# Kernel tuning notes

Hardware: AMD Instinct MI355X
Metric: run time of the kernel (lower is better)

Reference implementation:

```python
import jax, jax.numpy as jnp
import numpy as np

D_MODEL = 1024
NUM_HEADS_Q = 16
NUM_HEADS_KV = 1
D_HEAD = D_MODEL // NUM_HEADS_Q  # 64
KV_DIM = D_HEAD * NUM_HEADS_KV   # 64


def setup_inputs() -> dict:
    key = jax.random.key(0)
    ks = jax.random.split(key, 9)
    b, n = 4, 2048
    s_in = 1.0 / np.sqrt(D_MODEL)
    s_o = 1.0 / np.sqrt(D_MODEL)
    return {
        "x": jax.random.normal(ks[0], (b, n, D_MODEL), jnp.float32),
        # weights stored as [in, out] (= torch Linear weight transposed)
        "W_q": jax.random.uniform(ks[1], (D_MODEL, D_MODEL), jnp.float32, -s_in, s_in),
        "b_q": jax.random.uniform(ks[2], (D_MODEL,), jnp.float32, -s_in, s_in),
        "W_k": jax.random.uniform(ks[3], (D_MODEL, KV_DIM), jnp.float32, -s_in, s_in),
        "b_k": jax.random.uniform(ks[4], (KV_DIM,), jnp.float32, -s_in, s_in),
        "W_v": jax.random.uniform(ks[5], (D_MODEL, KV_DIM), jnp.float32, -s_in, s_in),
        "b_v": jax.random.uniform(ks[6], (KV_DIM,), jnp.float32, -s_in, s_in),
        "W_o": jax.random.uniform(ks[7], (D_MODEL, D_MODEL), jnp.float32, -s_o, s_o),
        "b_o": jax.random.uniform(ks[8], (D_MODEL,), jnp.float32, -s_o, s_o),
    }


def reference(x, W_q, b_q, W_k, b_k, W_v, b_v, W_o, b_o):
    b, n, d_model = x.shape
    # projections
    q = (x @ W_q + b_q).reshape(b, n, NUM_HEADS_Q, D_HEAD).transpose(0, 2, 1, 3)  # [b,hq,n,dh]
    k = (x @ W_k + b_k).reshape(b, n, NUM_HEADS_KV, D_HEAD).transpose(0, 2, 1, 3)  # [b,hkv,n,dh]
    v = (x @ W_v + b_v).reshape(b, n, NUM_HEADS_KV, D_HEAD).transpose(0, 2, 1, 3)
    # MQA: single KV head broadcast over query heads via einsum broadcasting
    scale = 1.0 / np.sqrt(D_HEAD).astype(np.float32)
    # scores [b,hq,n,n]; k/v have hkv=1, broadcast over hq
    scores = jnp.einsum("bhqd,bknd->bhqn", q, k)[..., 0, :, :][:, :, None] if False else None
    # cleaner: squeeze kv head (num_heads_kv == 1)
    k1 = k[:, 0]  # [b,n,dh]
    v1 = v[:, 0]  # [b,n,dh]
    scores = jnp.einsum("bhqd,bkd->bhqk", q, k1) * scale  # [b,hq,n,n]
    attn = jax.nn.softmax(scores, axis=-1)
    out = jnp.einsum("bhqk,bkd->bhqd", attn, v1)  # [b,hq,n,dh]
    out = out.transpose(0, 2, 1, 3).reshape(b, n, d_model)
    return out @ W_o + b_o
```

## Files before the change

### kernel.cpp

```cpp
#include <hip/hip_runtime.h>

using bf16x8 = __attribute__((ext_vector_type(8))) short;
using f32x4  = __attribute__((ext_vector_type(4))) float;
using f32x16 = __attribute__((ext_vector_type(16))) float;
using u32x2  = __attribute__((ext_vector_type(2))) unsigned int;
using u32x4  = __attribute__((ext_vector_type(4))) unsigned int;

__device__ __forceinline__ unsigned short f2bf(float f) {
  unsigned int u = __float_as_uint(f);
  u = u + 0x7fffu + ((u >> 16) & 1u);
  return (unsigned short)(u >> 16);
}

#if __has_builtin(__builtin_amdgcn_exp2f)
#define EXP2(x) __builtin_amdgcn_exp2f(x)
#else
#define EXP2(x) __expf((x) * 0.69314718056f)
#endif

__device__ __forceinline__ unsigned int cvt_pk_bf16(float lo, float hi) {
  unsigned int r;
  asm("v_cvt_pk_bf16_f32 %0, %1, %2" : "=v"(r) : "v"(lo), "v"(hi));
  return r;
}

#define GLL16(SRC, DST) __builtin_amdgcn_global_load_lds( \
    (const __attribute__((address_space(1))) unsigned int*)(SRC), \
    (__attribute__((address_space(3))) unsigned int*)(DST), 16, 0, 0)

__global__ void cvt_x_kernel(const float* __restrict__ x, unsigned short* __restrict__ xb, int n4) {
  int i = blockIdx.x * blockDim.x + threadIdx.x;
  if (i >= n4) return;
  const float4 v = reinterpret_cast<const float4*>(x)[i];
  ushort2 o0 = { f2bf(v.x), f2bf(v.y) };
  ushort2 o1 = { f2bf(v.z), f2bf(v.w) };
  reinterpret_cast<ushort2*>(xb)[2 * i]     = o0;
  reinterpret_cast<ushort2*>(xb)[2 * i + 1] = o1;
}

__global__ __launch_bounds__(256) void cvt_wt_kernel(
    const float* __restrict__ W, unsigned short* __restrict__ Wt, int N, int K) {
  __shared__ float tile[32][33];
  const int n0 = blockIdx.x * 32, k0 = blockIdx.y * 32;
  const int tx = threadIdx.x & 31, ty = threadIdx.x >> 5;
  #pragma unroll
  for (int i = 0; i < 32; i += 8)
    tile[ty + i][tx] = W[(size_t)(k0 + ty + i) * N + n0 + tx];
  __syncthreads();
  #pragma unroll
  for (int i = 0; i < 32; i += 8)
    Wt[(size_t)(n0 + ty + i) * K + k0 + tx] = f2bf(tile[tx][ty + i]);
}

template<int MODE>
__global__ __launch_bounds__(256) void gemm_kernel(
    const unsigned short* __restrict__ A, const unsigned short* __restrict__ Bt,
    const float* __restrict__ bias0, const float* __restrict__ bias1,
    const float* __restrict__ bias2,
    void* __restrict__ out0, void* __restrict__ out1, void* __restrict__ out2,
    int K, int N) {
  __shared__ __align__(16) unsigned short alds[2][128 * 32];
  __shared__ __align__(16) unsigned short blds[2][128 * 32];

  const int t    = threadIdx.x;
  const int lane = t & 63;
  const int wid  = t >> 6;
  const int lr = lane & 15, lg = lane >> 4;
  const int row0 = blockIdx.x * 128;
  const int col0 = blockIdx.y * 128;

  const size_t ldb = (size_t)K * 2;
  const char* Ag = (const char*)A  + (size_t)(row0 + (t >> 2)) * ldb + ((t & 3) << 4);
  const char* Bg = (const char*)Bt + (size_t)(col0 + (t >> 2)) * ldb + ((t & 3) << 4);
  char* adst = (char*)alds[0] + wid * 1024;
  char* bdst = (char*)blds[0] + wid * 1024;

  auto stage = [&](int buf, int k0) {
    const size_t kb = (size_t)k0 * 2;
    #pragma unroll
    for (int c = 0; c < 2; ++c) {
      GLL16(Ag + (size_t)c * 64 * ldb + kb, adst + buf * 8192 + c * 4096);
      GLL16(Bg + (size_t)c * 64 * ldb + kb, bdst + buf * 8192 + c * 4096);
    }
  };

  f32x4 acc[4][4];
  #pragma unroll
  for (int i = 0; i < 4; ++i)
    #pragma unroll
    for (int j = 0; j < 4; ++j)
      #pragma unroll
      for (int r = 0; r < 4; ++r) acc[i][j][r] = 0.f;

  stage(0, 0);
  __syncthreads();

  for (int step = 0; step < 32; ++step) {
    const int cur = step & 1;
    if (step < 31) stage(cur ^ 1, (step + 1) * 32);

    const char* ab = (const char*)alds[cur] + (wid >> 1) * 4096;
    const char* bb = (const char*)blds[cur] + (wid & 1) * 4096;
    bf16x8 am[4], bn[4];
    #pragma unroll
    for (int i = 0; i < 4; ++i)
      am[i] = *reinterpret_cast<const bf16x8*>(ab + (i * 16 + lr) * 64 + lg * 16);
    #pragma unroll
    for (int j = 0; j < 4; ++j)
      bn[j] = *reinterpret_cast<const bf16x8*>(bb + (j * 16 + lr) * 64 + lg * 16);
    #pragma unroll
    for (int i = 0; i < 4; ++i)
      #pragma unroll
      for (int j = 0; j < 4; ++j)
        acc[i][j] = __builtin_amdgcn_mfma_f32_16x16x32_bf16(am[i], bn[j], acc[i][j], 0, 0, 0);

    __syncthreads();
  }

  const int wrow0 = row0 + (wid >> 1) * 64;
  const int wcol0 = col0 + (wid & 1) * 64;
  #pragma unroll
  for (int i = 0; i < 4; ++i) {
    #pragma unroll
    for (int j = 0; j < 4; ++j) {
      const int col = wcol0 + j * 16 + lr;
      float bias;
      if constexpr (MODE == 0)
        bias = (col < 1024) ? bias0[col] : ((col < 1088) ? bias1[col - 1024] : bias2[col - 1088]);
      else
        bias = bias0[col];
      #pragma unroll
      for (int r = 0; r < 4; ++r) {
        const int row = wrow0 + i * 16 + lg * 4 + r;
        float v = acc[i][j][r] + bias;
        if constexpr (MODE == 0) {
          const int b = row >> 11, n = row & 2047;
          if (col < 1024) {
            v *= 0.180336880111f;
            const int h = col >> 6, d = col & 63;
            ((unsigned short*)out0)[(((b * 16 + h) * 2048) + n) * 64 + d] = f2bf(v);
          } else if (col < 1088) {
            ((unsigned short*)out1)[row * 64 + (col - 1024)] = f2bf(v);
          } else {
            const int np = (n & ~15) | (n & 3) | ((n & 4) << 1) | ((n & 8) >> 1);
            ((unsigned short*)out2)[(b * 64 + (col - 1088)) * 2048 + np] = f2bf(v);
          }
        } else {
          ((float*)out0)[(size_t)row * N + col] = v;
        }
      }
    }
  }
}

__global__ __launch_bounds__(512, 4) void attn_kernel(
    const unsigned short* __restrict__ Q,
    const unsigned short* __restrict__ Kb,
    const unsigned short* __restrict__ Vt,
    unsigned short* __restrict__ Ao) {
  __shared__ __align__(16) unsigned short klds[2][128 * 64];
  __shared__ __align__(16) unsigned short vlds[2][64 * 128];

  const int lane = threadIdx.x & 63;
  const int wid  = threadIdx.x >> 6;
  const int la = lane & 31, hi = lane >> 5;
  const int swz = (la & 7) << 4;
  const int bh = blockIdx.y, b = bh >> 4, h = bh & 15;
  const int q0 = blockIdx.x * 256 + wid * 32;

  const unsigned short* Qb = Q + (size_t)bh * 2048 * 64;
  const char* Kbase = (const char*)(Kb + (size_t)b * 2048 * 64);
  const char* Vbase = (const char*)(Vt + (size_t)b * 64 * 2048);

  const int srowK  = lane >> 3;
  const int schnkK = (lane & 7) ^ srowK;
  const int koff0 = (wid * 16 + 0 + srowK) * 128 + schnkK * 16;
  const int koff1 = (wid * 16 + 8 + srowK) * 128 + schnkK * 16;
  const int srowV = lane >> 4;
  const int voff0 = (wid * 8 + 0 + srowV) * 4096 + ((lane & 15) ^ ((0 + srowV) & 7)) * 16;
  const int voff1 = (wid * 8 + 4 + srowV) * 4096 + ((lane & 15) ^ ((4 + srowV) & 7)) * 16;
  char* kB = (char*)klds[0] + wid * 2048;
  char* vB = (char*)vlds[0] + wid * 2048;

  auto stage = [&](int buf, int p) {
    const size_t kgb = (size_t)p * 16384;
    const size_t vgb = (size_t)p * 256;
    GLL16(Kbase + kgb + koff0, kB + buf * 16384);
    GLL16(Kbase + kgb + koff1, kB + buf * 16384 + 1024);
    GLL16(Vbase + vgb + voff0, vB + buf * 16384);
    GLL16(Vbase + vgb + voff1, vB + buf * 16384 + 1024);
  };

  bf16x8 qa[4];
  #pragma unroll
  for (int kc = 0; kc < 4; ++kc)
    qa[kc] = *reinterpret_cast<const bf16x8*>(&Qb[(q0 + la) * 64 + kc * 16 + hi * 8]);

  float lsum = 0.f;
  f32x16 o[2];
  #pragma unroll
  for (int dt = 0; dt < 2; ++dt)
    #pragma unroll
    for (int r = 0; r < 16; ++r) o[dt][r] = 0.f;

  stage(0, 0);
  __syncthreads();

  for (int p = 0; p < 16; ++p) {
    const int cur = p & 1;
    if (p < 15) stage(cur ^ 1, p + 1);

    const char* kb8 = (const char*)klds[cur];
    const char* vb8 = (const char*)vlds[cur];

    #pragma unroll
    for (int ct = 0; ct < 4; ++ct) {
      f32x16 s;
      #pragma unroll
      for (int r = 0; r < 16; ++r) s[r] = 0.f;
      #pragma unroll
      for (int kc = 0; kc < 4; ++kc) {
        const bf16x8 kf = *reinterpret_cast<const bf16x8*>(
            kb8 + ((ct * 32 + la) << 7) + ((((kc << 1) + hi) << 4) ^ swz));
        s = __builtin_amdgcn_mfma_f32_32x32x16_bf16(kf, qa[kc], s, 0, 0, 0);
      }

      unsigned int W[4][2];
      float ps = 0.f;
      #pragma unroll
      for (int r2 = 0; r2 < 4; ++r2) {
        const float p0 = EXP2(s[r2 * 4 + 0]);
        const float p1 = EXP2(s[r2 * 4 + 1]);
        const float p2 = EXP2(s[r2 * 4 + 2]);
        const float p3 = EXP2(s[r2 * 4 + 3]);
        ps += (p0 + p1) + (p2 + p3);
        W[r2][0] = cvt_pk_bf16(p0, p1);
        W[r2][1] = cvt_pk_bf16(p2, p3);
      }
      lsum += ps;

      #pragma unroll
      for (int ks = 0; ks < 2; ++ks) {
        u32x4 pwv;
        pwv[0] = W[2 * ks][0];
        pwv[1] = W[2 * ks][1];
        pwv[2] = W[2 * ks + 1][0];
        pwv[3] = W[2 * ks + 1][1];
        const bf16x8 pb = __builtin_bit_cast(bf16x8, pwv);
        #pragma unroll
        for (int dt = 0; dt < 2; ++dt) {
          const bf16x8 vf = *reinterpret_cast<const bf16x8*>(
              vb8 + ((dt * 32 + la) << 8) + (((((ct * 2 + ks) << 1) + hi) << 4) ^ swz));
          o[dt] = __builtin_amdgcn_mfma_f32_32x32x16_bf16(vf, pb, o[dt], 0, 0, 0);
        }
      }
    }

    __syncthreads();
  }

  lsum += __shfl_xor(lsum, 32);
  const float inv = 1.f / lsum;
  const size_t rowoff = (size_t)(b * 2048 + q0 + la) * 1024 + h * 64 + hi * 4;
  #pragma unroll
  for (int dt = 0; dt < 2; ++dt) {
    #pragma unroll
    for (int r2 = 0; r2 < 4; ++r2) {
      u32x2 w;
      w[0] = cvt_pk_bf16(o[dt][r2 * 4 + 0] * inv, o[dt][r2 * 4 + 1] * inv);
      w[1] = cvt_pk_bf16(o[dt][r2 * 4 + 2] * inv, o[dt][r2 * 4 + 3] * inv);
      *(u32x2*)(Ao + rowoff + dt * 32 + r2 * 8) = w;
    }
  }
}

extern "C" void kernel_launch(void* const* d_in, const int* in_sizes, int n_in,
                              void* d_out, int out_size, void* d_ws, size_t ws_size,
                              hipStream_t stream) {
  const float* x  = (const float*)d_in[0];
  const float* Wq = (const float*)d_in[1];
  const float* bq = (const float*)d_in[2];
  const float* Wk = (const float*)d_in[3];
  const float* bk = (const float*)d_in[4];
  const float* Wv = (const float*)d_in[5];
  const float* bv = (const float*)d_in[6];
  const float* Wo = (const float*)d_in[7];
  const float* bo = (const float*)d_in[8];
  float* out = (float*)d_out;

  char* ws = (char*)d_ws;
  size_t off = 0;
  auto alloc = [&](size_t bytes) -> void* {
    void* p = ws + off;
    off += (bytes + 255) & ~(size_t)255;
    return p;
  };
  unsigned short* xb    = (unsigned short*)alloc((size_t)8192 * 1024 * 2);
  unsigned short* wqkvt = (unsigned short*)alloc((size_t)1152 * 1024 * 2);
  unsigned short* wot   = (unsigned short*)alloc((size_t)1024 * 1024 * 2);
  unsigned short* qb    = (unsigned short*)alloc((size_t)8192 * 1024 * 2);
  unsigned short* kb    = (unsigned short*)alloc((size_t)8192 * 64 * 2);
  unsigned short* vt    = (unsigned short*)alloc((size_t)4 * 64 * 2048 * 2);
  unsigned short* ao    = (unsigned short*)alloc((size_t)8192 * 1024 * 2);

  cvt_x_kernel<<<8192, 256, 0, stream>>>(x, xb, 8192 * 1024 / 4);
  cvt_wt_kernel<<<dim3(32, 32), 256, 0, stream>>>(Wq, wqkvt, 1024, 1024);
  cvt_wt_kernel<<<dim3(2, 32), 256, 0, stream>>>(Wk, wqkvt + (size_t)1024 * 1024, 64, 1024);
  cvt_wt_kernel<<<dim3(2, 32), 256, 0, stream>>>(Wv, wqkvt + (size_t)1088 * 1024, 64, 1024);
  cvt_wt_kernel<<<dim3(32, 32), 256, 0, stream>>>(Wo, wot, 1024, 1024);

  gemm_kernel<0><<<dim3(64, 9), 256, 0, stream>>>(xb, wqkvt, bq, bk, bv, qb, kb, vt, 1024, 1152);
  attn_kernel<<<dim3(8, 64), 512, 0, stream>>>(qb, kb, vt, ao);
  gemm_kernel<2><<<dim3(64, 8), 256, 0, stream>>>(ao, wot, bo, nullptr, nullptr, out, nullptr, nullptr, 1024, 1024);
}
```

Measured before the change: 161.5 us.

## Fuse conversion kernels, software-pipeline QK and PV with priorities, relax attention occupancy

The five fp32-to-bf16 conversion launches are merged into one kernel that dispatches on block index, removing launch overhead. Inside attention, the QK^T MFMA for the next column tile is issued before the exp/PV of the previous one, with s_setprio raised around MFMA bursts so matrix work overlaps the exp work of other waves. The launch-bounds minimum blocks is lowered from 4 to 2, letting the compiler use more registers for the extra live score tile, at the cost of possibly lower occupancy.

```diff
diff --git a/kernel.cpp b/kernel.cpp
--- a/kernel.cpp
+++ b/kernel.cpp
@@ -28,20 +28,29 @@
     (const __attribute__((address_space(1))) unsigned int*)(SRC), \
     (__attribute__((address_space(3))) unsigned int*)(DST), 16, 0, 0)
 
-__global__ void cvt_x_kernel(const float* __restrict__ x, unsigned short* __restrict__ xb, int n4) {
-  int i = blockIdx.x * blockDim.x + threadIdx.x;
-  if (i >= n4) return;
-  const float4 v = reinterpret_cast<const float4*>(x)[i];
-  ushort2 o0 = { f2bf(v.x), f2bf(v.y) };
-  ushort2 o1 = { f2bf(v.z), f2bf(v.w) };
-  reinterpret_cast<ushort2*>(xb)[2 * i]     = o0;
-  reinterpret_cast<ushort2*>(xb)[2 * i + 1] = o1;
-}
-
-__global__ __launch_bounds__(256) void cvt_wt_kernel(
-    const float* __restrict__ W, unsigned short* __restrict__ Wt, int N, int K) {
+__global__ __launch_bounds__(256) void cvt_all_kernel(
+    const float* __restrict__ x, unsigned short* __restrict__ xb,
+    const float* __restrict__ Wq, const float* __restrict__ Wk,
+    const float* __restrict__ Wv, const float* __restrict__ Wo,
+    unsigned short* __restrict__ wqkvt, unsigned short* __restrict__ wot) {
   __shared__ float tile[32][33];
-  const int n0 = blockIdx.x * 32, k0 = blockIdx.y * 32;
+  const int bx = blockIdx.x;
+  if (bx < 8192) {
+    const int i = bx * 256 + threadIdx.x;
+    const float4 v = reinterpret_cast<const float4*>(x)[i];
+    ushort2 o0 = { f2bf(v.x), f2bf(v.y) };
+    ushort2 o1 = { f2bf(v.z), f2bf(v.w) };
+    reinterpret_cast<ushort2*>(xb)[2 * i]     = o0;
+    reinterpret_cast<ushort2*>(xb)[2 * i + 1] = o1;
+    return;
+  }
+  const float* W; unsigned short* Wt; int N, bi;
+  if (bx < 9216)      { W = Wq; Wt = wqkvt;                        N = 1024; bi = bx - 8192; }
+  else if (bx < 9280) { W = Wk; Wt = wqkvt + (size_t)1024 * 1024;  N = 64;   bi = bx - 9216; }
+  else if (bx < 9344) { W = Wv; Wt = wqkvt + (size_t)1088 * 1024;  N = 64;   bi = bx - 9280; }
+  else                { W = Wo; Wt = wot;                          N = 1024; bi = bx - 9344; }
+  const int nb = N >> 5;
+  const int n0 = (bi % nb) * 32, k0 = (bi / nb) * 32;
   const int tx = threadIdx.x & 31, ty = threadIdx.x >> 5;
   #pragma unroll
   for (int i = 0; i < 32; i += 8)
@@ -49,7 +58,7 @@
   __syncthreads();
   #pragma unroll
   for (int i = 0; i < 32; i += 8)
-    Wt[(size_t)(n0 + ty + i) * K + k0 + tx] = f2bf(tile[tx][ty + i]);
+    Wt[(size_t)(n0 + ty + i) * 1024 + k0 + tx] = f2bf(tile[tx][ty + i]);
 }
 
 template<int MODE>
@@ -153,7 +162,7 @@
   }
 }
 
-__global__ __launch_bounds__(512, 4) void attn_kernel(
+__global__ __launch_bounds__(512, 2) void attn_kernel(
     const unsigned short* __restrict__ Q,
     const unsigned short* __restrict__ Kb,
     const unsigned short* __restrict__ Vt,
@@ -213,18 +222,22 @@
     const char* kb8 = (const char*)klds[cur];
     const char* vb8 = (const char*)vlds[cur];
 
-    #pragma unroll
-    for (int ct = 0; ct < 4; ++ct) {
+    auto QKc = [&](int ct) -> f32x16 {
       f32x16 s;
       #pragma unroll
       for (int r = 0; r < 16; ++r) s[r] = 0.f;
+      __builtin_amdgcn_s_setprio(1);
       #pragma unroll
       for (int kc = 0; kc < 4; ++kc) {
         const bf16x8 kf = *reinterpret_cast<const bf16x8*>(
             kb8 + ((ct * 32 + la) << 7) + ((((kc << 1) + hi) << 4) ^ swz));
         s = __builtin_amdgcn_mfma_f32_32x32x16_bf16(kf, qa[kc], s, 0, 0, 0);
       }
-
+      __builtin_amdgcn_s_setprio(0);
+      return s;
+    };
+
+    auto ExpPV = [&](int ct, const f32x16& s) {
       unsigned int W[4][2];
       float ps = 0.f;
       #pragma unroll
@@ -238,7 +251,7 @@
         W[r2][1] = cvt_pk_bf16(p2, p3);
       }
       lsum += ps;
-
+      __builtin_amdgcn_s_setprio(1);
       #pragma unroll
       for (int ks = 0; ks < 2; ++ks) {
         u32x4 pwv;
@@ -254,7 +267,17 @@
           o[dt] = __builtin_amdgcn_mfma_f32_32x32x16_bf16(vf, pb, o[dt], 0, 0, 0);
         }
       }
-    }
+      __builtin_amdgcn_s_setprio(0);
+    };
+
+    f32x16 s0 = QKc(0);
+    f32x16 s1 = QKc(1);
+    ExpPV(0, s0);
+    s0 = QKc(2);
+    ExpPV(1, s1);
+    s1 = QKc(3);
+    ExpPV(2, s0);
+    ExpPV(3, s1);
 
     __syncthreads();
   }
@@ -303,12 +326,7 @@
   unsigned short* vt    = (unsigned short*)alloc((size_t)4 * 64 * 2048 * 2);
   unsigned short* ao    = (unsigned short*)alloc((size_t)8192 * 1024 * 2);
 
-  cvt_x_kernel<<<8192, 256, 0, stream>>>(x, xb, 8192 * 1024 / 4);
-  cvt_wt_kernel<<<dim3(32, 32), 256, 0, stream>>>(Wq, wqkvt, 1024, 1024);
-  cvt_wt_kernel<<<dim3(2, 32), 256, 0, stream>>>(Wk, wqkvt + (size_t)1024 * 1024, 64, 1024);
-  cvt_wt_kernel<<<dim3(2, 32), 256, 0, stream>>>(Wv, wqkvt + (size_t)1088 * 1024, 64, 1024);
-  cvt_wt_kernel<<<dim3(32, 32), 256, 0, stream>>>(Wo, wot, 1024, 1024);
-
+  cvt_all_kernel<<<10368, 256, 0, stream>>>(x, xb, Wq, Wk, Wv, Wo, wqkvt, wot);
   gemm_kernel<0><<<dim3(64, 9), 256, 0, stream>>>(xb, wqkvt, bq, bk, bv, qb, kb, vt, 1024, 1152);
   attn_kernel<<<dim3(8, 64), 512, 0, stream>>>(qb, kb, vt, ao);
   gemm_kernel<2><<<dim3(64, 8), 256, 0, stream>>>(ao, wot, bo, nullptr, nullptr, out, nullptr, nullptr, 1024, 1024);
```

After: 151.7 us. 1.06x faster.
